# Kernel optimization log

Measured on AMD Instinct MI355X. Metric: run time of the kernel, lower is better.

The kernel has to match this reference:

```python
import jax, jax.numpy as jnp
import numpy as np
from functools import partial


def conv2d(x, w, b=None, stride=1):
    # torch Conv2d(k=3, padding=1, stride=stride), NCHW / OIHW
    y = jax.lax.conv_general_dilated(
        x, w, window_strides=(stride, stride), padding=((1, 1), (1, 1)),
        dimension_numbers=("NCHW", "OIHW", "NCHW"))
    if b is not None:
        y = y + b[None, :, None, None]
    return y


def conv_offset2d(x, ow):
    """ConvOffset2D: conv -> (B*C,H,W,2) offsets -> bilinear sample of x at grid+offset."""
    B, C, H, W = x.shape
    off = conv2d(x, ow)                      # (B, 2C, H, W), no bias
    off = off.reshape(B * C, H, W, 2)        # faithful raw reshape as in torch code
    xb = x.reshape(B * C, H, W)
    rr, cc = jnp.meshgrid(jnp.arange(H, dtype=x.dtype), jnp.arange(W, dtype=x.dtype), indexing="ij")
    r = jnp.clip(off[..., 0] + rr, 0.0, H - 1)   # row coords, clamped
    c = jnp.clip(off[..., 1] + cc, 0.0, W - 1)   # col coords, clamped
    r0 = jnp.floor(r); r1 = jnp.ceil(r)
    c0 = jnp.floor(c); c1 = jnp.ceil(c)
    bi = jnp.arange(B * C)[:, None, None]

    def gather(ri, ci):
        return xb[bi, ri.astype(jnp.int32), ci.astype(jnp.int32)]

    v_lt = gather(r0, c0)  # (floor r, floor c)
    v_rb = gather(r1, c1)  # (ceil r,  ceil c)
    v_lb = gather(r0, c1)  # (floor r, ceil c)
    v_rt = gather(r1, c0)  # (ceil r,  floor c)
    fr = r - r0
    fc = c - c0
    vt = v_lt + (v_rt - v_lt) * fr
    vb = v_lb + (v_rb - v_lb) * fr
    out = vt + (vb - vt) * fc
    return out.reshape(B, C, H, W)


def setup_inputs() -> dict:
    key = jax.random.key(0)
    ks = jax.random.split(key, 16)
    C = 32
    B, H, W = 16, 256, 256

    def conv_w(k, co, ci):
        return jax.random.normal(k, (co, ci, 3, 3), jnp.float32) * (1.0 / np.sqrt(ci * 9))

    inp = {
        "x": jax.random.normal(ks[0], (B, C, H, W), jnp.float32),
        "w1": conv_w(ks[1], C, C),       "b1": jnp.zeros((C,), jnp.float32),
        "ow1": jax.random.normal(ks[2], (2 * C, C, 3, 3), jnp.float32) * 0.01,
        "w2": conv_w(ks[3], 2 * C, C),   "b2": jnp.zeros((2 * C,), jnp.float32),
        "ow2": jax.random.normal(ks[4], (4 * C, 2 * C, 3, 3), jnp.float32) * 0.01,
        "w3": conv_w(ks[5], C, 2 * C),   "b3": jnp.zeros((C,), jnp.float32),
        "ow3": jax.random.normal(ks[6], (2 * C, C, 3, 3), jnp.float32) * 0.01,
        "w4": conv_w(ks[7], C, C),       "b4": jnp.zeros((C,), jnp.float32),
    }
    return inp


def reference(x, w1, b1, ow1, w2, b2, ow2, w3, b3, ow3, w4, b4):
    # Dropout layers are identity in eval mode.
    h = jax.nn.relu(conv2d(x, w1, b1))                 # (B, C, H, W)
    h = conv_offset2d(h, ow1)
    h = jax.nn.relu(conv2d(h, w2, b2, stride=2))       # (B, 2C, H/2, W/2)
    h = conv_offset2d(h, ow2)
    h = jax.nn.relu(conv2d(h, w3, b3, stride=2))       # (B, C, H/4, W/4)
    h = conv_offset2d(h, ow3)
    h = jax.nn.relu(conv2d(h, w4, b4, stride=2))       # (B, C, H/8, W/8)
    return jnp.mean(h, axis=(2, 3), keepdims=True)     # global avg pool -> (B, C, 1, 1)
```

## Files before the change

### kernel.cpp

```cpp
#include <hip/hip_runtime.h>

typedef short short8 __attribute__((ext_vector_type(8)));
typedef float f32x4 __attribute__((ext_vector_type(4)));

__device__ __forceinline__ unsigned short f2b(float f) {
    unsigned u = __float_as_uint(f);
    u += 0x7fffu + ((u >> 16) & 1u);
    return (unsigned short)(u >> 16);
}
__device__ __forceinline__ float b2f(unsigned short h) {
    return __uint_as_float(((unsigned)h) << 16);
}

template <int C_IN, int C_OUT, int NW, int DEFORM>
__global__ __launch_bounds__(NW * 64) void conv_s1_mfma(
    const unsigned short* __restrict__ in, const unsigned short* __restrict__ wT,
    const float* __restrict__ bias, unsigned short* __restrict__ out,
    int H, int W, int relu)
{
    constexpr int LDSTR  = C_IN + 8;
    constexpr int KSTEPS = C_IN / 32;
    constexpr int CH8    = C_IN / 8;
    constexpr int COPB   = 32 * (NW / 4);
    static_assert(!DEFORM || COPB == 64, "deform fusion expects 64 conv ch/block");
    constexpr int S_IN   = 18 * 18 * LDSTR;
    constexpr int S_OFF  = DEFORM ? 16 * 16 * 64 : 0;
    constexpr int SMEM   = (S_IN > S_OFF) ? S_IN : S_OFF;
    __shared__ __align__(16) unsigned short s_in[SMEM];

    const int tid   = threadIdx.x;
    const int wave  = tid >> 6;
    const int wv    = wave & 3;
    const int csub  = wave >> 2;
    const int lane  = tid & 63;
    const int mlane = lane & 15;
    const int quad  = lane >> 4;

    const int nCo  = C_OUT / COPB;
    const int b    = blockIdx.z / nCo;
    const int coB  = (blockIdx.z - b * nCo) * COPB + csub * 32;
    const int row0 = blockIdx.y * 16;
    const int col0 = blockIdx.x * 16;

    for (int idx = tid; idx < 18 * 18 * CH8; idx += NW * 64) {
        int pixel = idx / CH8;
        int ch    = (idx - pixel * CH8) * 8;
        int pr    = pixel / 18;
        int pc    = pixel - pr * 18;
        int gr = row0 - 1 + pr, gc = col0 - 1 + pc;
        ulonglong2 v; v.x = 0; v.y = 0;
        if ((unsigned)gr < (unsigned)H && (unsigned)gc < (unsigned)W)
            v = *(const ulonglong2*)&in[((b * H + gr) * W + gc) * C_IN + ch];
        *(ulonglong2*)&s_in[pixel * LDSTR + ch] = v;
    }
    __syncthreads();

    f32x4 acc[2][4];
    #pragma unroll
    for (int mt = 0; mt < 2; ++mt)
        #pragma unroll
        for (int t = 0; t < 4; ++t) acc[mt][t] = (f32x4)(0.f);

    #pragma unroll 1
    for (int kk = 0; kk < KSTEPS; ++kk) {
        short8 A[2][9];
        #pragma unroll
        for (int mt = 0; mt < 2; ++mt)
            #pragma unroll
            for (int tap = 0; tap < 9; ++tap)
                A[mt][tap] = *(const short8*)&wT[(tap * C_OUT + coB + mt * 16 + mlane) * C_IN
                                                 + kk * 32 + quad * 8];

        const unsigned short* sb =
            &s_in[(wv * 4 * 18 + mlane) * LDSTR + kk * 32 + quad * 8];
        #pragma unroll
        for (int t = 0; t < 4; ++t) {
            #pragma unroll
            for (int tap = 0; tap < 9; ++tap) {
                const int dy = tap / 3, dx = tap % 3;
                short8 Bf = *(const short8*)&sb[((t + dy) * 18 + dx) * LDSTR];
                acc[0][t] = __builtin_amdgcn_mfma_f32_16x16x32_bf16(A[0][tap], Bf, acc[0][t], 0, 0, 0);
                acc[1][t] = __builtin_amdgcn_mfma_f32_16x16x32_bf16(A[1][tap], Bf, acc[1][t], 0, 0, 0);
            }
        }
    }

    if (!DEFORM) {
        #pragma unroll
        for (int mt = 0; mt < 2; ++mt) {
            const int cb = coB + mt * 16 + quad * 4;
            float4 bv;
            if (bias) bv = *(const float4*)&bias[cb]; else { bv.x = bv.y = bv.z = bv.w = 0.f; }
            #pragma unroll
            for (int t = 0; t < 4; ++t) {
                const int row = row0 + wv * 4 + t, col = col0 + mlane;
                float o0 = acc[mt][t][0] + bv.x, o1 = acc[mt][t][1] + bv.y;
                float o2 = acc[mt][t][2] + bv.z, o3 = acc[mt][t][3] + bv.w;
                if (relu) {
                    o0 = fmaxf(o0, 0.f); o1 = fmaxf(o1, 0.f);
                    o2 = fmaxf(o2, 0.f); o3 = fmaxf(o3, 0.f);
                }
                ushort4 pk; pk.x = f2b(o0); pk.y = f2b(o1); pk.z = f2b(o2); pk.w = f2b(o3);
                *(ushort4*)&out[((b * H + row) * W + col) * C_OUT + cb] = pk;
            }
        }
    } else {
        __syncthreads();
        #pragma unroll
        for (int mt = 0; mt < 2; ++mt) {
            const int cb  = csub * 32 + mt * 16 + quad * 4;
            const int swc = cb ^ ((mlane & 7) << 3);
            #pragma unroll
            for (int t = 0; t < 4; ++t) {
                ushort4 pk;
                pk.x = f2b(acc[mt][t][0]); pk.y = f2b(acc[mt][t][1]);
                pk.z = f2b(acc[mt][t][2]); pk.w = f2b(acc[mt][t][3]);
                *(ushort4*)&s_in[((wv * 4 + t) * 16 + mlane) * 64 + swc] = pk;
            }
        }
        __syncthreads();

        const int ci   = tid & 31;
        const int slot = tid >> 5;
        const int zb   = blockIdx.z - b * nCo;
        const int xch  = zb * 32 + ci;
        const int Hh = H >> 1, Wh = W >> 1;
        const int r8 = blockIdx.y * 8, c8 = blockIdx.x * 8;
        const unsigned short* xb = in  + (long)b * H * W * C_IN + xch;
        unsigned short*       ob = out + (long)b * H * W * C_IN + xch;
        const float Hm1 = (float)(H - 1), Wm1 = (float)(W - 1);
        const int drC = W * C_IN, dcC = C_IN;

        #pragma unroll 2
        for (int s = 0; s < 8; ++s) {
            const int pos = slot + s * 16;
            const int rl  = pos >> 4;
            const int cl  = (pos >> 1) & 7;
            const int chf = pos & 1;
            const int lr  = rl * 2 + chf;
            const int lc  = cl * 2;
            const int bix = (lr * 16 + lc) * 64;
            const ushort2 roP = *(const ushort2*)&s_in[bix +      ((2 * ci) ^ ((lc & 7) << 3))];
            const ushort2 coP = *(const ushort2*)&s_in[bix + 64 + ((2 * ci) ^ (((lc + 1) & 7) << 3))];
            const int rg = r8 + rl;
            const int cg = c8 + cl + chf * Wh;
            #pragma unroll
            for (int ih = 0; ih < 2; ++ih) {
                const int rowg = ih ? rg + Hh : rg;
                const float rr = fminf(fmaxf(b2f(ih ? roP.y : roP.x) + (float)rowg, 0.f), Hm1);
                const float cc = fminf(fmaxf(b2f(ih ? coP.y : coP.x) + (float)cg,   0.f), Wm1);
                const float rf = floorf(rr), cf = floorf(cc);
                const float fr = rr - rf,  fc = cc - cf;
                const int idx00 = ((int)rf * W + (int)cf) * C_IN;
                const int dr = (fr > 0.f) ? drC : 0;
                const int dc = (fc > 0.f) ? dcC : 0;
                const float v00 = b2f(xb[idx00]);
                const float v01 = b2f(xb[idx00 + dc]);
                const float v10 = b2f(xb[idx00 + dr]);
                const float v11 = b2f(xb[idx00 + dr + dc]);
                const float vt = v00 + (v10 - v00) * fr;
                const float vb = v01 + (v11 - v01) * fr;
                const float rs = vt + (vb - vt) * fc;
                ob[(rowg * W + cg) * C_IN] = f2b(rs);
            }
        }
    }
}

template <int C_IN, int C_OUT, int NW>
__global__ __launch_bounds__(NW * 64) void conv_s2_mfma(
    const unsigned short* __restrict__ in, const unsigned short* __restrict__ wT,
    const float* __restrict__ bias, unsigned short* __restrict__ out,
    int H_in, int W_in, int relu)
{
    constexpr int LDSTR  = C_IN + 8;
    constexpr int KSTEPS = C_IN / 32;
    constexpr int CH8    = C_IN / 8;
    constexpr int COPB   = 32 * (NW / 4);
    __shared__ unsigned short s_in[17 * 17 * LDSTR];

    const int tid   = threadIdx.x;
    const int wave  = tid >> 6;
    const int wv    = wave & 3;
    const int csub  = wave >> 2;
    const int lane  = tid & 63;
    const int mlane = lane & 15;
    const int quad  = lane >> 4;

    const int H_out = H_in >> 1, W_out = W_in >> 1;
    const int nCo   = C_OUT / COPB;
    const int b     = blockIdx.z / nCo;
    const int coB   = (blockIdx.z - b * nCo) * COPB + csub * 32;
    const int orow0 = blockIdx.y * 8, ocol0 = blockIdx.x * 8;
    const int irow0 = orow0 * 2 - 1,  icol0 = ocol0 * 2 - 1;

    for (int idx = tid; idx < 17 * 17 * CH8; idx += NW * 64) {
        int pixel = idx / CH8;
        int ch    = (idx - pixel * CH8) * 8;
        int pr    = pixel / 17;
        int pc    = pixel - pr * 17;
        int gr = irow0 + pr, gc = icol0 + pc;
        ulonglong2 v; v.x = 0; v.y = 0;
        if ((unsigned)gr < (unsigned)H_in && (unsigned)gc < (unsigned)W_in)
            v = *(const ulonglong2*)&in[((b * H_in + gr) * W_in + gc) * C_IN + ch];
        *(ulonglong2*)&s_in[pixel * LDSTR + ch] = v;
    }
    __syncthreads();

    f32x4 acc[2];
    acc[0] = (f32x4)(0.f); acc[1] = (f32x4)(0.f);

    const int plr = wv * 2 + (mlane >> 3);
    const int plc = mlane & 7;

    #pragma unroll 1
    for (int kk = 0; kk < KSTEPS; ++kk) {
        short8 A[2][9];
        #pragma unroll
        for (int mt = 0; mt < 2; ++mt)
            #pragma unroll
            for (int tap = 0; tap < 9; ++tap)
                A[mt][tap] = *(const short8*)&wT[(tap * C_OUT + coB + mt * 16 + mlane) * C_IN
                                                 + kk * 32 + quad * 8];

        const unsigned short* sb0 =
            &s_in[(plr * 2 * 17 + plc * 2) * LDSTR + kk * 32 + quad * 8];
        #pragma unroll
        for (int tap = 0; tap < 9; ++tap) {
            const int dy = tap / 3, dx = tap % 3;
            short8 Bf = *(const short8*)&sb0[(dy * 17 + dx) * LDSTR];
            acc[0] = __builtin_amdgcn_mfma_f32_16x16x32_bf16(A[0][tap], Bf, acc[0], 0, 0, 0);
            acc[1] = __builtin_amdgcn_mfma_f32_16x16x32_bf16(A[1][tap], Bf, acc[1], 0, 0, 0);
        }
    }

    const int row = orow0 + plr, col = ocol0 + plc;
    #pragma unroll
    for (int mt = 0; mt < 2; ++mt) {
        const int cb = coB + mt * 16 + quad * 4;
        float4 bv;
        if (bias) bv = *(const float4*)&bias[cb]; else { bv.x = bv.y = bv.z = bv.w = 0.f; }
        float o0 = acc[mt][0] + bv.x, o1 = acc[mt][1] + bv.y;
        float o2 = acc[mt][2] + bv.z, o3 = acc[mt][3] + bv.w;
        if (relu) {
            o0 = fmaxf(o0, 0.f); o1 = fmaxf(o1, 0.f);
            o2 = fmaxf(o2, 0.f); o3 = fmaxf(o3, 0.f);
        }
        ushort4 pk; pk.x = f2b(o0); pk.y = f2b(o1); pk.z = f2b(o2); pk.w = f2b(o3);
        *(ushort4*)&out[((b * H_out + row) * W_out + col) * C_OUT + cb] = pk;
    }
}

__global__ __launch_bounds__(256) void nchw2nhwc(
    const float* __restrict__ x, unsigned short* __restrict__ out, int HW)
{
    __shared__ float s[32][65];
    const int b = blockIdx.y, p0 = blockIdx.x * 64;
    const int tid = threadIdx.x;
    #pragma unroll
    for (int k = 0; k < 8; ++k) {
        int e = tid + k * 256, ci = e >> 6, p = e & 63;
        s[ci][p] = x[(b * 32 + ci) * HW + p0 + p];
    }
    __syncthreads();
    #pragma unroll
    for (int k = 0; k < 8; ++k) {
        int e = tid + k * 256, p = e >> 5, ci = e & 31;
        out[(b * HW + p0 + p) * 32 + ci] = f2b(s[ci][p]);
    }
}

struct WTArgs {
    const float* src[7];
    unsigned short* dst[7];
    int co[7], ci[7], n[7];
};
__global__ __launch_bounds__(256) void wtrans_all(WTArgs a)
{
    const int i = blockIdx.x * 256 + threadIdx.x;
    #pragma unroll
    for (int s = 0; s < 7; ++s) {
        if (i < a.n[s]) {
            const int ci  = i % a.ci[s];
            const int rr  = i / a.ci[s];
            const int co  = rr % a.co[s];
            const int tap = rr / a.co[s];
            a.dst[s][i] = f2b(a.src[s][(co * a.ci[s] + ci) * 9 + tap]);
        }
    }
}

__global__ __launch_bounds__(256) void avgpool_nhwc(
    const unsigned short* __restrict__ in, float* __restrict__ out)
{
    const int b = blockIdx.x, tid = threadIdx.x;
    const int ci = tid & 31, pg = tid >> 5;
    float s = 0.f;
    for (int k = 0; k < 128; ++k) {
        int p = pg * 128 + k;
        s += b2f(in[(b * 1024 + p) * 32 + ci]);
    }
    __shared__ float red[8][32];
    red[pg][ci] = s;
    __syncthreads();
    if (tid < 32) {
        float t = 0.f;
        #pragma unroll
        for (int j = 0; j < 8; ++j) t += red[j][tid];
        out[b * 32 + tid] = t * (1.f / 1024.f);
    }
}

__global__ __launch_bounds__(256) void sentinel(float* out, int n, float v)
{
    int i = blockIdx.x * 256 + threadIdx.x;
    if (i < n) out[i] = v;
}

extern "C" void kernel_launch(void* const* d_in, const int* in_sizes, int n_in,
                              void* d_out, int out_size, void* d_ws, size_t ws_size,
                              hipStream_t stream) {
    (void)in_sizes; (void)n_in; (void)out_size;
    const float* x   = (const float*)d_in[0];
    const float* w1  = (const float*)d_in[1];
    const float* b1  = (const float*)d_in[2];
    const float* ow1 = (const float*)d_in[3];
    const float* w2  = (const float*)d_in[4];
    const float* b2  = (const float*)d_in[5];
    const float* ow2 = (const float*)d_in[6];
    const float* w3  = (const float*)d_in[7];
    const float* b3  = (const float*)d_in[8];
    const float* ow3 = (const float*)d_in[9];
    const float* w4  = (const float*)d_in[10];
    const float* b4  = (const float*)d_in[11];
    float* out = (float*)d_out;
    unsigned short* wsu = (unsigned short*)d_ws;

    const size_t XB = 0;
    const size_t HA = 33554432;
    const size_t OB = 67108864;
    const size_t DC = 134217728;
    const size_t WB = 167772160;
    const size_t total_us = WB + 165888;
    if (ws_size < total_us * 2) {
        sentinel<<<2, 256, 0, stream>>>(out, 512, 12345.0f);
        return;
    }
    (void)OB;
    unsigned short* xb = wsu + XB;
    unsigned short* hA = wsu + HA;
    unsigned short* dC = wsu + DC;
    unsigned short* wt1  = wsu + WB;
    unsigned short* owt1 = wt1 + 9216;
    unsigned short* wt2  = owt1 + 18432;
    unsigned short* owt2 = wt2 + 18432;
    unsigned short* wt3  = owt2 + 73728;
    unsigned short* owt3 = wt3 + 18432;
    unsigned short* wt4  = owt3 + 18432;

    WTArgs wa;
    wa.src[0] = w1;  wa.dst[0] = wt1;  wa.co[0] = 32;  wa.ci[0] = 32; wa.n[0] = 9216;
    wa.src[1] = ow1; wa.dst[1] = owt1; wa.co[1] = 64;  wa.ci[1] = 32; wa.n[1] = 18432;
    wa.src[2] = w2;  wa.dst[2] = wt2;  wa.co[2] = 64;  wa.ci[2] = 32; wa.n[2] = 18432;
    wa.src[3] = ow2; wa.dst[3] = owt2; wa.co[3] = 128; wa.ci[3] = 64; wa.n[3] = 73728;
    wa.src[4] = w3;  wa.dst[4] = wt3;  wa.co[4] = 32;  wa.ci[4] = 64; wa.n[4] = 18432;
    wa.src[5] = ow3; wa.dst[5] = owt3; wa.co[5] = 64;  wa.ci[5] = 32; wa.n[5] = 18432;
    wa.src[6] = w4;  wa.dst[6] = wt4;  wa.co[6] = 32;  wa.ci[6] = 32; wa.n[6] = 9216;
    wtrans_all<<<288, 256, 0, stream>>>(wa);

    nchw2nhwc<<<dim3(1024, 16), 256, 0, stream>>>(x, xb, 65536);

    conv_s1_mfma<32, 32, 4, 0><<<dim3(16, 16, 16), 256, 0, stream>>>(xb, wt1, b1, hA, 256, 256, 1);
    conv_s1_mfma<32, 64, 8, 1><<<dim3(16, 16, 16), 512, 0, stream>>>(hA, owt1, nullptr, dC, 256, 256, 0);

    conv_s2_mfma<32, 64, 8><<<dim3(16, 16, 16), 512, 0, stream>>>(dC, wt2, b2, hA, 256, 256, 1);
    conv_s1_mfma<64, 128, 8, 1><<<dim3(8, 8, 32), 512, 0, stream>>>(hA, owt2, nullptr, dC, 128, 128, 0);

    conv_s2_mfma<64, 32, 4><<<dim3(8, 8, 16), 256, 0, stream>>>(dC, wt3, b3, hA, 128, 128, 1);
    conv_s1_mfma<32, 64, 8, 1><<<dim3(4, 4, 16), 512, 0, stream>>>(hA, owt3, nullptr, dC, 64, 64, 0);

    conv_s2_mfma<32, 32, 4><<<dim3(4, 4, 16), 256, 0, stream>>>(dC, wt4, b4, hA, 64, 64, 1);
    avgpool_nhwc<<<16, 256, 0, stream>>>(hA, out);
}
```

Measured before the change: 607.9 us.

## Emit planar copy of conv outputs for paired bilinear gathers in deform

Conv kernels feeding a deformable sampling stage now also write a channel-planar (NCHW) bf16 copy of their output. The deform stage reads from that planar copy, fetching two adjacent columns per row with one 8-byte load plus alignbit, so each sample needs two loads instead of four strided NHWC gathers. The thread mapping and LDS swizzle for the offset tile are reworked so each thread handles one channel/half and lanes share a channel. This trades extra scattered 2-byte stores and extra memory traffic in the producer convs for cheaper, more local gathers.

New measurement: 674.0 us. +10.9%, slower.

```diff
diff --git a/kernel.cpp b/kernel.cpp
--- a/kernel.cpp
+++ b/kernel.cpp
@@ -2,6 +2,7 @@
 
 typedef short short8 __attribute__((ext_vector_type(8)));
 typedef float f32x4 __attribute__((ext_vector_type(4)));
+typedef unsigned int u32x2 __attribute__((ext_vector_type(2)));
 
 __device__ __forceinline__ unsigned short f2b(float f) {
     unsigned u = __float_as_uint(f);
@@ -12,10 +13,11 @@
     return __uint_as_float(((unsigned)h) << 16);
 }
 
-template <int C_IN, int C_OUT, int NW, int DEFORM>
+template <int C_IN, int C_OUT, int NW, int DEFORM, int POUT>
 __global__ __launch_bounds__(NW * 64) void conv_s1_mfma(
     const unsigned short* __restrict__ in, const unsigned short* __restrict__ wT,
     const float* __restrict__ bias, unsigned short* __restrict__ out,
+    const unsigned short* __restrict__ inp, unsigned short* __restrict__ outp,
     int H, int W, int relu)
 {
     constexpr int LDSTR  = C_IN + 8;
@@ -86,6 +88,7 @@
     }
 
     if (!DEFORM) {
+        const int HW = H * W;
         #pragma unroll
         for (int mt = 0; mt < 2; ++mt) {
             const int cb = coB + mt * 16 + quad * 4;
@@ -102,14 +105,21 @@
                 }
                 ushort4 pk; pk.x = f2b(o0); pk.y = f2b(o1); pk.z = f2b(o2); pk.w = f2b(o3);
                 *(ushort4*)&out[((b * H + row) * W + col) * C_OUT + cb] = pk;
+                if (POUT) {
+                    const int pbase = ((b * C_OUT + cb) * H + row) * W + col;
+                    outp[pbase]          = pk.x;
+                    outp[pbase + HW]     = pk.y;
+                    outp[pbase + 2 * HW] = pk.z;
+                    outp[pbase + 3 * HW] = pk.w;
+                }
             }
         }
     } else {
         __syncthreads();
         #pragma unroll
         for (int mt = 0; mt < 2; ++mt) {
-            const int cb  = csub * 32 + mt * 16 + quad * 4;
-            const int swc = cb ^ ((mlane & 7) << 3);
+            const int cb4 = csub * 32 + mt * 16 + quad * 4;
+            const int swc = cb4 ^ ((mlane & 15) << 2);
             #pragma unroll
             for (int t = 0; t < 4; ++t) {
                 ushort4 pk;
@@ -120,57 +130,56 @@
         }
         __syncthreads();
 
-        const int ci   = tid & 31;
-        const int slot = tid >> 5;
-        const int zb   = blockIdx.z - b * nCo;
-        const int xch  = zb * 32 + ci;
+        const int zb  = blockIdx.z - b * nCo;
+        const int ci  = (wave & 3) * 8 + (lane >> 3);
+        const int cl  = lane & 7;
+        const int ih  = wave >> 2;
+        const int xch = zb * 32 + ci;
         const int Hh = H >> 1, Wh = W >> 1;
         const int r8 = blockIdx.y * 8, c8 = blockIdx.x * 8;
-        const unsigned short* xb = in  + (long)b * H * W * C_IN + xch;
+        const unsigned short* xp = inp + (long)(b * C_IN + xch) * (H * W);
         unsigned short*       ob = out + (long)b * H * W * C_IN + xch;
         const float Hm1 = (float)(H - 1), Wm1 = (float)(W - 1);
-        const int drC = W * C_IN, dcC = C_IN;
-
-        #pragma unroll 2
-        for (int s = 0; s < 8; ++s) {
-            const int pos = slot + s * 16;
-            const int rl  = pos >> 4;
-            const int cl  = (pos >> 1) & 7;
-            const int chf = pos & 1;
+        const int cho = 2 * ci + ih;
+        const int lc  = cl * 2;
+
+        #pragma unroll 4
+        for (int u = 0; u < 16; ++u) {
+            const int rl  = u >> 1;
+            const int chf = u & 1;
             const int lr  = rl * 2 + chf;
-            const int lc  = cl * 2;
-            const int bix = (lr * 16 + lc) * 64;
-            const ushort2 roP = *(const ushort2*)&s_in[bix +      ((2 * ci) ^ ((lc & 7) << 3))];
-            const ushort2 coP = *(const ushort2*)&s_in[bix + 64 + ((2 * ci) ^ (((lc + 1) & 7) << 3))];
-            const int rg = r8 + rl;
-            const int cg = c8 + cl + chf * Wh;
-            #pragma unroll
-            for (int ih = 0; ih < 2; ++ih) {
-                const int rowg = ih ? rg + Hh : rg;
-                const float rr = fminf(fmaxf(b2f(ih ? roP.y : roP.x) + (float)rowg, 0.f), Hm1);
-                const float cc = fminf(fmaxf(b2f(ih ? coP.y : coP.x) + (float)cg,   0.f), Wm1);
-                const float rf = floorf(rr), cf = floorf(cc);
-                const float fr = rr - rf,  fc = cc - cf;
-                const int idx00 = ((int)rf * W + (int)cf) * C_IN;
-                const int dr = (fr > 0.f) ? drC : 0;
-                const int dc = (fc > 0.f) ? dcC : 0;
-                const float v00 = b2f(xb[idx00]);
-                const float v01 = b2f(xb[idx00 + dc]);
-                const float v10 = b2f(xb[idx00 + dr]);
-                const float v11 = b2f(xb[idx00 + dr + dc]);
-                const float vt = v00 + (v10 - v00) * fr;
-                const float vb = v01 + (v11 - v01) * fr;
-                const float rs = vt + (vb - vt) * fc;
-                ob[(rowg * W + cg) * C_IN] = f2b(rs);
-            }
-        }
-    }
-}
-
-template <int C_IN, int C_OUT, int NW>
+            const unsigned short ro = s_in[(lr * 16 + lc    ) * 64 + (cho ^ ((lc & 15) << 2))];
+            const unsigned short co = s_in[(lr * 16 + lc + 1) * 64 + (cho ^ (((lc + 1) & 15) << 2))];
+            const int rowg = r8 + rl + ih * Hh;
+            const int cg   = c8 + cl + chf * Wh;
+            const float rr = fminf(fmaxf(b2f(ro) + (float)rowg, 0.f), Hm1);
+            const float cc = fminf(fmaxf(b2f(co) + (float)cg,   0.f), Wm1);
+            const float rf = floorf(rr), cf = floorf(cc);
+            const float fr = rr - rf,  fc = cc - cf;
+            const int idx00 = (int)rf * W + (int)cf;
+            const int idx10 = idx00 + ((fr > 0.f) ? W : 0);
+            const int sh = (idx00 & 1) << 4;
+            const u32x2 dA = *(const u32x2*)(xp + (idx00 & ~1));
+            const u32x2 dB = *(const u32x2*)(xp + (idx10 & ~1));
+            const unsigned qA = __builtin_amdgcn_alignbit(dA.y, dA.x, sh);
+            const unsigned qB = __builtin_amdgcn_alignbit(dB.y, dB.x, sh);
+            const float v00 = __uint_as_float(qA << 16);
+            const float v01 = __uint_as_float(qA & 0xffff0000u);
+            const float v10 = __uint_as_float(qB << 16);
+            const float v11 = __uint_as_float(qB & 0xffff0000u);
+            const float vt = v00 + (v10 - v00) * fr;
+            const float vb = v01 + (v11 - v01) * fr;
+            const float rs = vt + (vb - vt) * fc;
+            ob[(rowg * W + cg) * C_IN] = f2b(rs);
+        }
+    }
+}
+
+template <int C_IN, int C_OUT, int NW, int POUT>
 __global__ __launch_bounds__(NW * 64) void conv_s2_mfma(
     const unsigned short* __restrict__ in, const unsigned short* __restrict__ wT,
     const float* __restrict__ bias, unsigned short* __restrict__ out,
+    unsigned short* __restrict__ outp,
     int H_in, int W_in, int relu)
 {
     constexpr int LDSTR  = C_IN + 8;
@@ -235,6 +244,7 @@
     }
 
     const int row = orow0 + plr, col = ocol0 + plc;
+    const int HWo = H_out * W_out;
     #pragma unroll
     for (int mt = 0; mt < 2; ++mt) {
         const int cb = coB + mt * 16 + quad * 4;
@@ -248,6 +258,13 @@
         }
         ushort4 pk; pk.x = f2b(o0); pk.y = f2b(o1); pk.z = f2b(o2); pk.w = f2b(o3);
         *(ushort4*)&out[((b * H_out + row) * W_out + col) * C_OUT + cb] = pk;
+        if (POUT) {
+            const int pbase = ((b * C_OUT + cb) * H_out + row) * W_out + col;
+            outp[pbase]           = pk.x;
+            outp[pbase + HWo]     = pk.y;
+            outp[pbase + 2 * HWo] = pk.z;
+            outp[pbase + 3 * HWo] = pk.w;
+        }
     }
 }
 
@@ -338,7 +355,7 @@
 
     const size_t XB = 0;
     const size_t HA = 33554432;
-    const size_t OB = 67108864;
+    const size_t PB = 67108864;
     const size_t DC = 134217728;
     const size_t WB = 167772160;
     const size_t total_us = WB + 165888;
@@ -346,10 +363,10 @@
         sentinel<<<2, 256, 0, stream>>>(out, 512, 12345.0f);
         return;
     }
-    (void)OB;
-    unsigned short* xb = wsu + XB;
-    unsigned short* hA = wsu + HA;
-    unsigned short* dC = wsu + DC;
+    unsigned short* xb  = wsu + XB;
+    unsigned short* hA  = wsu + HA;
+    unsigned short* hAp = wsu + PB;
+    unsigned short* dC  = wsu + DC;
     unsigned short* wt1  = wsu + WB;
     unsigned short* owt1 = wt1 + 9216;
     unsigned short* wt2  = owt1 + 18432;
@@ -370,15 +387,22 @@
 
     nchw2nhwc<<<dim3(1024, 16), 256, 0, stream>>>(x, xb, 65536);
 
-    conv_s1_mfma<32, 32, 4, 0><<<dim3(16, 16, 16), 256, 0, stream>>>(xb, wt1, b1, hA, 256, 256, 1);
-    conv_s1_mfma<32, 64, 8, 1><<<dim3(16, 16, 16), 512, 0, stream>>>(hA, owt1, nullptr, dC, 256, 256, 0);
-
-    conv_s2_mfma<32, 64, 8><<<dim3(16, 16, 16), 512, 0, stream>>>(dC, wt2, b2, hA, 256, 256, 1);
-    conv_s1_mfma<64, 128, 8, 1><<<dim3(8, 8, 32), 512, 0, stream>>>(hA, owt2, nullptr, dC, 128, 128, 0);
-
-    conv_s2_mfma<64, 32, 4><<<dim3(8, 8, 16), 256, 0, stream>>>(dC, wt3, b3, hA, 128, 128, 1);
-    conv_s1_mfma<32, 64, 8, 1><<<dim3(4, 4, 16), 512, 0, stream>>>(hA, owt3, nullptr, dC, 64, 64, 0);
-
-    conv_s2_mfma<32, 32, 4><<<dim3(4, 4, 16), 256, 0, stream>>>(dC, wt4, b4, hA, 64, 64, 1);
+    conv_s1_mfma<32, 32, 4, 0, 1><<<dim3(16, 16, 16), 256, 0, stream>>>(
+        xb, wt1, b1, hA, nullptr, hAp, 256, 256, 1);
+    conv_s1_mfma<32, 64, 8, 1, 0><<<dim3(16, 16, 16), 512, 0, stream>>>(
+        hA, owt1, nullptr, dC, hAp, nullptr, 256, 256, 0);
+
+    conv_s2_mfma<32, 64, 8, 1><<<dim3(16, 16, 16), 512, 0, stream>>>(
+        dC, wt2, b2, hA, hAp, 256, 256, 1);
+    conv_s1_mfma<64, 128, 8, 1, 0><<<dim3(8, 8, 32), 512, 0, stream>>>(
+        hA, owt2, nullptr, dC, hAp, nullptr, 128, 128, 0);
+
+    conv_s2_mfma<64, 32, 4, 1><<<dim3(8, 8, 16), 256, 0, stream>>>(
+        dC, wt3, b3, hA, hAp, 128, 128, 1);
+    conv_s1_mfma<32, 64, 8, 1, 0><<<dim3(4, 4, 16), 512, 0, stream>>>(
+        hA, owt3, nullptr, dC, hAp, nullptr, 64, 64, 0);
+
+    conv_s2_mfma<32, 32, 4, 0><<<dim3(4, 4, 16), 256, 0, stream>>>(
+        dC, wt4, b4, hA, nullptr, 64, 64, 1);
     avgpool_nhwc<<<16, 256, 0, stream>>>(hA, out);
 }
```

## Stage deform sampling neighborhoods in LDS with global fallback for far offsets

Applied to the files above, without the earlier changes.

In the fused deformable-sampling epilogue, offsets now go to a separate LDS buffer. The conv input buffer is reused to hold four 10x10x32 halo tiles around each sample region. Bilinear taps that land inside a staged tile read from LDS; the rest fall back to global gathers. This is meant to cut scattered global memory traffic, since offsets are small and samples stay near their grid point. The cost is more LDS per block, which may lower occupancy, plus an extra cooperative load and a divergent branch. The sample loop unroll also goes from 2 to 4.

After: 559.6 us. 7.9% less time.

```diff
diff --git a/kernel.cpp b/kernel.cpp
--- a/kernel.cpp
+++ b/kernel.cpp
@@ -23,10 +23,10 @@
     constexpr int CH8    = C_IN / 8;
     constexpr int COPB   = 32 * (NW / 4);
     static_assert(!DEFORM || COPB == 64, "deform fusion expects 64 conv ch/block");
-    constexpr int S_IN   = 18 * 18 * LDSTR;
-    constexpr int S_OFF  = DEFORM ? 16 * 16 * 64 : 0;
-    constexpr int SMEM   = (S_IN > S_OFF) ? S_IN : S_OFF;
-    __shared__ __align__(16) unsigned short s_in[SMEM];
+    constexpr int S_IN = 18 * 18 * LDSTR;
+    static_assert(!DEFORM || S_IN >= 4 * 100 * 32, "sample buffer must fit in s_in");
+    __shared__ __align__(16) unsigned short s_in[S_IN];
+    __shared__ __align__(16) unsigned short s_off[DEFORM ? 16 * 16 * 64 : 8];
 
     const int tid   = threadIdx.x;
     const int wave  = tid >> 6;
@@ -105,7 +105,13 @@
             }
         }
     } else {
+        const int zb    = blockIdx.z - b * nCo;
+        const int zbase = zb * 32;
+        const int Hh = H >> 1, Wh = W >> 1;
+        const int r8 = blockIdx.y * 8, c8 = blockIdx.x * 8;
+
         __syncthreads();
+
         #pragma unroll
         for (int mt = 0; mt < 2; ++mt) {
             const int cb  = csub * 32 + mt * 16 + quad * 4;
@@ -115,23 +121,33 @@
                 ushort4 pk;
                 pk.x = f2b(acc[mt][t][0]); pk.y = f2b(acc[mt][t][1]);
                 pk.z = f2b(acc[mt][t][2]); pk.w = f2b(acc[mt][t][3]);
-                *(ushort4*)&s_in[((wv * 4 + t) * 16 + mlane) * 64 + swc] = pk;
+                *(ushort4*)&s_off[((wv * 4 + t) * 16 + mlane) * 64 + swc] = pk;
             }
+        }
+
+        for (int idx = tid; idx < 1600; idx += NW * 64) {
+            const int pixel = idx >> 2;
+            const int chq   = (idx & 3) * 8;
+            const int reg   = pixel / 100;
+            const int rem   = pixel - reg * 100;
+            const int rr_   = rem / 10;
+            const int cc_   = rem - rr_ * 10;
+            int gr = r8 + (reg >> 1) * Hh - 1 + rr_;
+            int gc = c8 + (reg & 1)  * Wh - 1 + cc_;
+            gr = gr < 0 ? 0 : (gr > H - 1 ? H - 1 : gr);
+            gc = gc < 0 ? 0 : (gc > W - 1 ? W - 1 : gc);
+            *(ulonglong2*)&s_in[pixel * 32 + chq] =
+                *(const ulonglong2*)&in[((b * H + gr) * W + gc) * C_IN + zbase + chq];
         }
         __syncthreads();
 
         const int ci   = tid & 31;
         const int slot = tid >> 5;
-        const int zb   = blockIdx.z - b * nCo;
-        const int xch  = zb * 32 + ci;
-        const int Hh = H >> 1, Wh = W >> 1;
-        const int r8 = blockIdx.y * 8, c8 = blockIdx.x * 8;
-        const unsigned short* xb = in  + (long)b * H * W * C_IN + xch;
-        unsigned short*       ob = out + (long)b * H * W * C_IN + xch;
+        const unsigned short* xb = in  + (long)b * H * W * C_IN + zbase + ci;
+        unsigned short*       ob = out + (long)b * H * W * C_IN + zbase + ci;
         const float Hm1 = (float)(H - 1), Wm1 = (float)(W - 1);
-        const int drC = W * C_IN, dcC = C_IN;
-
-        #pragma unroll 2
+
+        #pragma unroll 4
         for (int s = 0; s < 8; ++s) {
             const int pos = slot + s * 16;
             const int rl  = pos >> 4;
@@ -140,24 +156,39 @@
             const int lr  = rl * 2 + chf;
             const int lc  = cl * 2;
             const int bix = (lr * 16 + lc) * 64;
-            const ushort2 roP = *(const ushort2*)&s_in[bix +      ((2 * ci) ^ ((lc & 7) << 3))];
-            const ushort2 coP = *(const ushort2*)&s_in[bix + 64 + ((2 * ci) ^ (((lc + 1) & 7) << 3))];
-            const int rg = r8 + rl;
-            const int cg = c8 + cl + chf * Wh;
+            const ushort2 roP = *(const ushort2*)&s_off[bix +      ((2 * ci) ^ ((lc & 7) << 3))];
+            const ushort2 coP = *(const ushort2*)&s_off[bix + 64 + ((2 * ci) ^ (((lc + 1) & 7) << 3))];
             #pragma unroll
             for (int ih = 0; ih < 2; ++ih) {
-                const int rowg = ih ? rg + Hh : rg;
+                const int R0 = r8 + ih * Hh, C0 = c8 + chf * Wh;
+                const int rowg = R0 + rl, cg = C0 + cl;
                 const float rr = fminf(fmaxf(b2f(ih ? roP.y : roP.x) + (float)rowg, 0.f), Hm1);
                 const float cc = fminf(fmaxf(b2f(ih ? coP.y : coP.x) + (float)cg,   0.f), Wm1);
                 const float rf = floorf(rr), cf = floorf(cc);
-                const float fr = rr - rf,  fc = cc - cf;
-                const int idx00 = ((int)rf * W + (int)cf) * C_IN;
-                const int dr = (fr > 0.f) ? drC : 0;
-                const int dc = (fc > 0.f) ? dcC : 0;
-                const float v00 = b2f(xb[idx00]);
-                const float v01 = b2f(xb[idx00 + dc]);
-                const float v10 = b2f(xb[idx00 + dr]);
-                const float v11 = b2f(xb[idx00 + dr + dc]);
+                const float fr = rr - rf, fc = cc - cf;
+                const int irf = (int)rf, icf = (int)cf;
+                const int dr1 = (fr > 0.f) ? 1 : 0;
+                const int dc1 = (fc > 0.f) ? 1 : 0;
+                const int lr0 = irf - R0 + 1;
+                const int lc0 = icf - C0 + 1;
+                float v00, v01, v10, v11;
+                if ((unsigned)lr0 <= (unsigned)(9 - dr1) &&
+                    (unsigned)lc0 <= (unsigned)(9 - dc1)) {
+                    const int reg = ih * 2 + chf;
+                    const unsigned short* sp =
+                        &s_in[(reg * 100 + lr0 * 10 + lc0) * 32 + ci];
+                    v00 = b2f(sp[0]);
+                    v01 = b2f(sp[dc1 * 32]);
+                    v10 = b2f(sp[dr1 * 320]);
+                    v11 = b2f(sp[dr1 * 320 + dc1 * 32]);
+                } else {
+                    const int idx00 = (irf * W + icf) * C_IN;
+                    const int dr = dr1 * W * C_IN, dc = dc1 * C_IN;
+                    v00 = b2f(xb[idx00]);
+                    v01 = b2f(xb[idx00 + dc]);
+                    v10 = b2f(xb[idx00 + dr]);
+                    v11 = b2f(xb[idx00 + dr + dc]);
+                }
                 const float vt = v00 + (v10 - v00) * fr;
                 const float vb = v01 + (v11 - v01) * fr;
                 const float rs = vt + (vb - vt) * fc;
@@ -338,7 +369,6 @@
 
     const size_t XB = 0;
     const size_t HA = 33554432;
-    const size_t OB = 67108864;
     const size_t DC = 134217728;
     const size_t WB = 167772160;
     const size_t total_us = WB + 165888;
@@ -346,7 +376,6 @@
         sentinel<<<2, 256, 0, stream>>>(out, 512, 12345.0f);
         return;
     }
-    (void)OB;
     unsigned short* xb = wsu + XB;
     unsigned short* hA = wsu + HA;
     unsigned short* dC = wsu + DC;
```
